# Optimization experiments

Measured on AMD Instinct MI355X. Metric: run time of the kernel, lower is better.

## Reference

```python
import jax, jax.numpy as jnp
import numpy as np

B, S = 128, 4096            # batch, num memory slots
W_NUM = 10000               # word_num (vocab)
CONT, FEAT, LSTM = 256, 256, 256
AH, CH = 128, 128           # actor/critic hidden dims
EPS = 1e-8


def _lin(key, out_d, in_d):
    k1, k2 = jax.random.split(key)
    s = 1.0 / np.sqrt(in_d)
    W = jax.random.uniform(k1, (out_d, in_d), jnp.float32, -s, s)
    b = jax.random.uniform(k2, (out_d,), jnp.float32, -s, s)
    return W, b


def setup_inputs() -> dict:
    key = jax.random.key(0)
    ks = jax.random.split(key, 18)
    d = {}
    d['x'] = jax.random.normal(ks[0], (B, W_NUM), jnp.float32)
    d['feat'] = jax.random.normal(ks[1], (B, S, FEAT), jnp.float32)
    d['h_tm1'] = jax.random.normal(ks[2], (B, LSTM), jnp.float32)
    d['c_tm1'] = jax.random.normal(ks[3], (B, LSTM), jnp.float32)
    d['W_x2cont'], d['b_x2cont'] = _lin(ks[4], CONT, W_NUM)
    d['W_h2cont'], d['b_h2cont'] = _lin(ks[5], CONT, LSTM)
    d['W_cont2key'], d['b_cont2key'] = _lin(ks[6], FEAT, CONT)
    d['W_cont2strength'], d['b_cont2strength'] = _lin(ks[7], 1, CONT)
    d['W_att_gates'], d['b_att_gates'] = _lin(ks[8], 1, FEAT + LSTM + CONT)
    d['W_ih'], d['b_ih'] = _lin(ks[9], 4 * LSTM, CONT + FEAT)
    d['W_hh'], d['b_hh'] = _lin(ks[10], 4 * LSTM, LSTM)
    d['W_actor_hid'], d['b_actor_hid'] = _lin(ks[11], AH, LSTM)
    d['W_critic_hid'], d['b_critic_hid'] = _lin(ks[12], CH, LSTM)
    d['W_actor'], d['b_actor'] = _lin(ks[13], W_NUM, AH)
    d['W_critic'], d['b_critic'] = _lin(ks[14], 1, CH)
    return d


def reference(x, feat, h_tm1, c_tm1,
              W_x2cont, b_x2cont, W_h2cont, b_h2cont,
              W_cont2key, b_cont2key, W_cont2strength, b_cont2strength,
              W_att_gates, b_att_gates, W_ih, b_ih, W_hh, b_hh,
              W_actor_hid, b_actor_hid, W_critic_hid, b_critic_hid,
              W_actor, b_actor, W_critic, b_critic):
    lin = lambda v, W, b: v @ W.T + b
    # controller
    x_cont = lin(x, W_x2cont, b_x2cont)                      # [B, CONT]
    h_cont = lin(h_tm1, W_h2cont, b_h2cont)                  # [B, CONT]
    control = jax.nn.relu(x_cont + h_cont)
    key_v = jnp.tanh(lin(control, W_cont2key, b_cont2key))   # [B, FEAT]
    strength = jax.nn.relu(lin(control, W_cont2strength, b_cont2strength)) + 1.0  # [B,1]
    # NTM-style content addressing: sharpened cosine similarity -> softmax over slots
    feat_n = jnp.linalg.norm(feat, axis=-1)                  # [B, S]
    key_n = jnp.linalg.norm(key_v, axis=-1, keepdims=True)   # [B, 1]
    sim = jnp.einsum('bsd,bd->bs', feat, key_v) / (feat_n * key_n + EPS)
    alpha = jax.nn.softmax(strength * sim, axis=-1)          # [B, S]
    cand_att_vec = jnp.einsum('bs,bsd->bd', alpha, feat)     # [B, FEAT]
    # attention gate
    gate_in = jnp.concatenate([cand_att_vec, h_tm1, x_cont], axis=1)  # [B, FEAT+LSTM+CONT]
    gates_att = jax.nn.sigmoid(lin(gate_in, W_att_gates, b_att_gates))
    att_vec = cand_att_vec * gates_att
    # LSTM cell (PyTorch gate order: i, f, g, o)
    inp_lstm = jnp.concatenate([att_vec, x_cont], axis=1)    # [B, FEAT+CONT]
    g = lin(inp_lstm, W_ih, b_ih) + lin(h_tm1, W_hh, b_hh)
    i, f, gg, o = jnp.split(g, 4, axis=1)
    c = jax.nn.sigmoid(f) * c_tm1 + jax.nn.sigmoid(i) * jnp.tanh(gg)
    h = jax.nn.sigmoid(o) * jnp.tanh(c)
    # heads
    action_logit = lin(jax.nn.relu(lin(h, W_actor_hid, b_actor_hid)), W_actor, b_actor)
    value = lin(jax.nn.relu(lin(h, W_critic_hid, b_critic_hid)), W_critic, b_critic)
    return (action_logit, value, h, c)
```

## Files before the change

kernel.cpp:

```cpp
#include <hip/hip_runtime.h>
#include <cmath>


#define B_ 128
#define S_ 4096
#define WN 10000
#define CD 256

__global__ __launch_bounds__(256) void k1_xcont(
    const float* __restrict__ x, const float* __restrict__ Wx,
    float* __restrict__ part) {
  const int nt = blockIdx.x;
  const int ks = blockIdx.y;
  const int t = threadIdx.x;
  __shared__ float4 xs[128][16];
  __shared__ float4 wsW[16][16];
  const int o0 = nt * 16;
  const int og = t & 3;
  const int bg = t >> 2;
  const int bgx = bg & 7;
  float acc[2][4] = {{0.f, 0.f, 0.f, 0.f}, {0.f, 0.f, 0.f, 0.f}};
  for (int sub = 0; sub < 4; ++sub) {
    const int k0 = ks * 256 + sub * 64;
    for (int q = t; q < 2048; q += 256) {
      const int row = q >> 4, c4 = q & 15;
      const int k = k0 + c4 * 4;
      float4 v = make_float4(0.f, 0.f, 0.f, 0.f);
      if (k < WN) v = *(const float4*)(x + (size_t)row * WN + k);
      xs[row][c4 ^ (row & 7)] = v;
    }
    {
      const int row = t >> 4, c4 = t & 15;
      const int k = k0 + c4 * 4;
      float4 v = make_float4(0.f, 0.f, 0.f, 0.f);
      if (k < WN) v = *(const float4*)(Wx + (size_t)(o0 + row) * WN + k);
      wsW[row][c4 ^ (row & 7)] = v;
    }
    __syncthreads();
#pragma unroll
    for (int c4 = 0; c4 < 16; ++c4) {
      float4 wv[4];
#pragma unroll
      for (int i = 0; i < 4; ++i) wv[i] = wsW[og * 4 + i][c4 ^ ((og * 4 + i) & 7)];
#pragma unroll
      for (int j = 0; j < 2; ++j) {
        const float4 xv = xs[bg + j * 64][c4 ^ bgx];
#pragma unroll
        for (int i = 0; i < 4; ++i)
          acc[j][i] += xv.x * wv[i].x + xv.y * wv[i].y + xv.z * wv[i].z + xv.w * wv[i].w;
      }
    }
    __syncthreads();
  }
#pragma unroll
  for (int j = 0; j < 2; ++j) {
    const int bb = bg + j * 64;
#pragma unroll
    for (int i = 0; i < 4; ++i)
      part[(size_t)ks * 32768 + bb * 256 + o0 + og * 4 + i] = acc[j][i];
  }
}

__global__ __launch_bounds__(256) void k2_controller(
    const float* __restrict__ part, const float* __restrict__ bx,
    const float* __restrict__ h_tm1, const float* __restrict__ Wh,
    const float* __restrict__ bh, const float* __restrict__ Wk,
    const float* __restrict__ bk, const float* __restrict__ Ws,
    const float* __restrict__ bs, float* __restrict__ x_cont,
    float* __restrict__ key_v, float* __restrict__ strength,
    float* __restrict__ key_n) {
  const int b = blockIdx.x, t = threadIdx.x;
  __shared__ float hs[256], cs[256];
  __shared__ float r1[4], r2[4];
  hs[t] = h_tm1[b * 256 + t];
  float xc = bx[t];
  for (int ks = 0; ks < 40; ++ks) xc += part[(size_t)ks * 32768 + b * 256 + t];
  x_cont[b * 256 + t] = xc;
  __syncthreads();
  float hc = bh[t];
  {
    const float* w = Wh + (size_t)t * 256;
    for (int k = 0; k < 256; k += 4) {
      float4 wv = *(const float4*)(w + k);
      hc += hs[k] * wv.x + hs[k + 1] * wv.y + hs[k + 2] * wv.z + hs[k + 3] * wv.w;
    }
  }
  const float ctl = fmaxf(xc + hc, 0.f);
  cs[t] = ctl;
  __syncthreads();
  float kvv = bk[t];
  {
    const float* w = Wk + (size_t)t * 256;
    for (int k = 0; k < 256; k += 4) {
      float4 wv = *(const float4*)(w + k);
      kvv += cs[k] * wv.x + cs[k + 1] * wv.y + cs[k + 2] * wv.z + cs[k + 3] * wv.w;
    }
  }
  kvv = tanhf(kvv);
  key_v[b * 256 + t] = kvv;
  float v1 = kvv * kvv;
  float v2 = ctl * Ws[t];
  for (int off = 32; off; off >>= 1) {
    v1 += __shfl_xor(v1, off);
    v2 += __shfl_xor(v2, off);
  }
  const int w_ = t >> 6, lane = t & 63;
  if (lane == 0) { r1[w_] = v1; r2[w_] = v2; }
  __syncthreads();
  if (t == 0) {
    const float n2 = r1[0] + r1[1] + r1[2] + r1[3];
    const float sd = r2[0] + r2[1] + r2[2] + r2[3];
    key_n[b] = sqrtf(n2);
    strength[b] = fmaxf(sd + bs[0], 0.f) + 1.f;
  }
}

__global__ __launch_bounds__(256, 4) void k3_attn(
    const float* __restrict__ feat, const float* __restrict__ key_v,
    const float* __restrict__ strength, const float* __restrict__ key_n,
    float* __restrict__ att_part) {
  const int ss = blockIdx.x;
  const int b = blockIdx.y;
  const int t = threadIdx.x;
  const int w = t >> 6, lane = t & 63;
  const int g = lane >> 4;
  const int l = lane & 15;
  const float str = strength[b];
  const float kn = key_n[b];
  float4 kf[4];
#pragma unroll
  for (int p = 0; p < 4; ++p)
    kf[p] = *(const float4*)(key_v + b * 256 + p * 64 + l * 4);
  const float* fb = feat + ((size_t)b * S_ + (size_t)ss * 256 + (size_t)w * 64) * 256;
  const float* fl = fb + (size_t)g * 256 + l * 4;
  float4 o[4];
#pragma unroll
  for (int p = 0; p < 4; ++p) o[p] = make_float4(0.f, 0.f, 0.f, 0.f);
  float lsum = 0.f;
  float4 fC[4], fN[4];
#pragma unroll
  for (int p = 0; p < 4; ++p) fC[p] = *(const float4*)(fl + p * 64);
#pragma unroll 2
  for (int r = 0; r < 16; ++r) {
    if (r < 15) {
      const float* fr = fl + (size_t)(r + 1) * 1024;
#pragma unroll
      for (int p = 0; p < 4; ++p) fN[p] = *(const float4*)(fr + p * 64);
    }
    float d = 0.f, n2 = 0.f;
#pragma unroll
    for (int p = 0; p < 4; ++p) {
      d  += fC[p].x * kf[p].x + fC[p].y * kf[p].y + fC[p].z * kf[p].z + fC[p].w * kf[p].w;
      n2 += fC[p].x * fC[p].x + fC[p].y * fC[p].y + fC[p].z * fC[p].z + fC[p].w * fC[p].w;
    }
#pragma unroll
    for (int off = 8; off; off >>= 1) {
      d  += __shfl_xor(d, off);
      n2 += __shfl_xor(n2, off);
    }
    const float sc = str * d / (sqrtf(n2) * kn + 1e-8f);
    const float a = __expf(sc - str);
    lsum += a;
#pragma unroll
    for (int p = 0; p < 4; ++p) {
      o[p].x += a * fC[p].x; o[p].y += a * fC[p].y;
      o[p].z += a * fC[p].z; o[p].w += a * fC[p].w;
    }
#pragma unroll
    for (int p = 0; p < 4; ++p) fC[p] = fN[p];
  }
#pragma unroll
  for (int off = 16; off <= 32; off <<= 1) {
    lsum += __shfl_xor(lsum, off);
#pragma unroll
    for (int p = 0; p < 4; ++p) {
      o[p].x += __shfl_xor(o[p].x, off);
      o[p].y += __shfl_xor(o[p].y, off);
      o[p].z += __shfl_xor(o[p].z, off);
      o[p].w += __shfl_xor(o[p].w, off);
    }
  }
  __shared__ float wo[4][256];
  __shared__ float wl[4];
  if (g == 0) {
#pragma unroll
    for (int p = 0; p < 4; ++p) *(float4*)&wo[w][p * 64 + l * 4] = o[p];
    if (l == 0) wl[w] = lsum;
  }
  __syncthreads();
  const float od = wo[0][t] + wo[1][t] + wo[2][t] + wo[3][t];
  float* apo = att_part + (size_t)(b * 16 + ss) * 264;
  if (t == 0) apo[0] = wl[0] + wl[1] + wl[2] + wl[3];
  apo[4 + t] = od;
}

__global__ __launch_bounds__(256) void k4a_gate(
    const float* __restrict__ att_part, const float* __restrict__ h_tm1,
    const float* __restrict__ x_cont, const float* __restrict__ Wg,
    const float* __restrict__ bg_, float* __restrict__ inp_cat) {
  const int b = blockIdx.x, t = threadIdx.x;
  const float* ap = att_part + (size_t)b * 16 * 264;
  float lg = 0.f, od = 0.f;
#pragma unroll
  for (int ss = 0; ss < 16; ++ss) {
    lg += ap[ss * 264];
    od += ap[ss * 264 + 4 + t];
  }
  const float cand = od / lg;
  const float hv = h_tm1[b * 256 + t];
  const float xc = x_cont[b * 256 + t];
  float v = cand * Wg[t] + hv * Wg[256 + t] + xc * Wg[512 + t];
  for (int off = 32; off; off >>= 1) v += __shfl_xor(v, off);
  __shared__ float rr[4];
  __shared__ float gsh;
  const int w_ = t >> 6, lane = t & 63;
  if (lane == 0) rr[w_] = v;
  __syncthreads();
  if (t == 0) {
    const float s = rr[0] + rr[1] + rr[2] + rr[3] + bg_[0];
    gsh = 1.f / (1.f + expf(-s));
  }
  __syncthreads();
  inp_cat[b * 768 + t] = cand * gsh;
  inp_cat[b * 768 + 256 + t] = xc;
  inp_cat[b * 768 + 512 + t] = hv;
}

__global__ __launch_bounds__(256) void k4b_lstm(
    const float* __restrict__ inp_cat, const float* __restrict__ Wih,
    const float* __restrict__ bih, const float* __restrict__ Whh,
    const float* __restrict__ bhh, const float* __restrict__ c_tm1,
    float* __restrict__ h_out, float* __restrict__ c_out) {
  const int j0 = blockIdx.x * 2;
  const int t = threadIdx.x;
  __shared__ float inp_s[128][132];
  __shared__ float w_s[8][132];
  const int b = t >> 1, half = t & 1;
  float acc[4] = {0.f, 0.f, 0.f, 0.f};
  for (int kc = 0; kc < 6; ++kc) {
    const int kbase = kc * 128;
    for (int q = t; q < 4096; q += 256) {
      const int row = q >> 5, c4 = q & 31;
      *(float4*)&inp_s[row][c4 * 4] =
          *(const float4*)(inp_cat + (size_t)row * 768 + kbase + c4 * 4);
    }
    {
      const int row = t >> 5, c4 = t & 31;
      const int gate = row & 3;
      const int j = j0 + (row >> 2);
      const int og = gate * 256 + j;
      const int kg = kbase + c4 * 4;
      float4 v;
      if (kg < 512) v = *(const float4*)(Wih + (size_t)og * 512 + kg);
      else          v = *(const float4*)(Whh + (size_t)og * 256 + (kg - 512));
      *(float4*)&w_s[row][c4 * 4] = v;
    }
    __syncthreads();
    for (int k = 0; k < 128; k += 4) {
      const float4 iv = *(const float4*)&inp_s[b][k];
#pragma unroll
      for (int g = 0; g < 4; ++g) {
        const float4 wv = *(const float4*)&w_s[half * 4 + g][k];
        acc[g] += iv.x * wv.x + iv.y * wv.y + iv.z * wv.z + iv.w * wv.w;
      }
    }
    __syncthreads();
  }
  const int j = j0 + half;
  const float gi = acc[0] + bih[j] + bhh[j];
  const float gf = acc[1] + bih[256 + j] + bhh[256 + j];
  const float gg = acc[2] + bih[512 + j] + bhh[512 + j];
  const float go = acc[3] + bih[768 + j] + bhh[768 + j];
  const float ct = c_tm1[b * 256 + j];
  const float i_ = 1.f / (1.f + expf(-gi));
  const float f_ = 1.f / (1.f + expf(-gf));
  const float g_ = tanhf(gg);
  const float o_ = 1.f / (1.f + expf(-go));
  const float c = f_ * ct + i_ * g_;
  const float h = o_ * tanhf(c);
  h_out[b * 256 + j] = h;
  c_out[b * 256 + j] = c;
}

__global__ __launch_bounds__(256) void k5_hid(
    const float* __restrict__ h_in, const float* __restrict__ Wah,
    const float* __restrict__ bah, const float* __restrict__ Wch,
    const float* __restrict__ bch, float* __restrict__ hidA,
    float* __restrict__ hidC) {
  const int b = blockIdx.x, t = threadIdx.x;
  __shared__ float hs[256];
  hs[t] = h_in[b * 256 + t];
  __syncthreads();
  const float* W = (t < 128) ? (Wah + (size_t)t * 256) : (Wch + (size_t)(t - 128) * 256);
  float s = (t < 128) ? bah[t] : bch[t - 128];
  for (int k = 0; k < 256; k += 4) {
    const float4 w = *(const float4*)(W + k);
    s += hs[k] * w.x + hs[k + 1] * w.y + hs[k + 2] * w.z + hs[k + 3] * w.w;
  }
  s = fmaxf(s, 0.f);
  if (t < 128) hidA[b * 128 + t] = s;
  else         hidC[b * 128 + (t - 128)] = s;
}

__global__ __launch_bounds__(256) void k6_heads(
    const float* __restrict__ hidA, const float* __restrict__ hidC,
    const float* __restrict__ Wa, const float* __restrict__ ba,
    const float* __restrict__ Wc, const float* __restrict__ bc,
    float* __restrict__ logits, float* __restrict__ value) {
  const int t = threadIdx.x;
  const int bx = blockIdx.x, by = blockIdx.y;
  if (bx == 157) {
    if (by == 0 && t < 128) {
      const float* hc = hidC + (size_t)t * 128;
      float s = bc[0];
      for (int k = 0; k < 128; k += 4) {
        const float4 w = *(const float4*)(Wc + k);
        s += hc[k] * w.x + hc[k + 1] * w.y + hc[k + 2] * w.z + hc[k + 3] * w.w;
      }
      value[t] = s;
    }
    return;
  }
  const int o0 = bx * 64;
  const int b0 = by * 32;
  __shared__ float4 ha[32][32];
  __shared__ float4 wa[64][32];
  for (int q = t; q < 1024; q += 256) {
    const int row = q >> 5, c4 = q & 31;
    ha[row][c4 ^ ((row >> 2) & 7)] =
        *(const float4*)(hidA + (size_t)(b0 + row) * 128 + c4 * 4);
  }
  for (int q = t; q < 2048; q += 256) {
    const int row = q >> 5, c4 = q & 31;
    const int o = o0 + row;
    float4 v = make_float4(0.f, 0.f, 0.f, 0.f);
    if (o < WN) v = *(const float4*)(Wa + (size_t)o * 128 + c4 * 4);
    wa[row][c4 ^ ((row >> 2) & 7)] = v;
  }
  __syncthreads();
  const int og = t & 15, bq = t >> 4;
  float acc[2][4];
#pragma unroll
  for (int r = 0; r < 2; ++r)
#pragma unroll
    for (int i = 0; i < 4; ++i) acc[r][i] = 0.f;
#pragma unroll 4
  for (int c4 = 0; c4 < 32; ++c4) {
    float4 wv[4];
#pragma unroll
    for (int i = 0; i < 4; ++i) wv[i] = wa[og * 4 + i][c4 ^ (og & 7)];
#pragma unroll
    for (int r = 0; r < 2; ++r) {
      const int row = bq * 2 + r;
      const float4 hv = ha[row][c4 ^ ((row >> 2) & 7)];
#pragma unroll
      for (int i = 0; i < 4; ++i)
        acc[r][i] += hv.x * wv[i].x + hv.y * wv[i].y + hv.z * wv[i].z + hv.w * wv[i].w;
    }
  }
  const int obase = o0 + og * 4;
#pragma unroll
  for (int r = 0; r < 2; ++r) {
    const int bb = b0 + bq * 2 + r;
    if (obase + 3 < WN) {
      const float4 bias = *(const float4*)(ba + obase);
      float4 res;
      res.x = acc[r][0] + bias.x;
      res.y = acc[r][1] + bias.y;
      res.z = acc[r][2] + bias.z;
      res.w = acc[r][3] + bias.w;
      *(float4*)(logits + (size_t)bb * WN + obase) = res;
    } else {
      for (int i = 0; i < 4; ++i)
        if (obase + i < WN) logits[(size_t)bb * WN + obase + i] = acc[r][i] + ba[obase + i];
    }
  }
}

extern "C" void kernel_launch(void* const* d_in, const int* in_sizes, int n_in,
                              void* d_out, int out_size, void* d_ws, size_t ws_size,
                              hipStream_t stream) {
  const float* x     = (const float*)d_in[0];
  const float* feat  = (const float*)d_in[1];
  const float* h_tm1 = (const float*)d_in[2];
  const float* c_tm1 = (const float*)d_in[3];
  const float* Wx2c  = (const float*)d_in[4];
  const float* bx2c  = (const float*)d_in[5];
  const float* Wh2c  = (const float*)d_in[6];
  const float* bh2c  = (const float*)d_in[7];
  const float* Wc2k  = (const float*)d_in[8];
  const float* bc2k  = (const float*)d_in[9];
  const float* Wc2s  = (const float*)d_in[10];
  const float* bc2s  = (const float*)d_in[11];
  const float* Wag   = (const float*)d_in[12];
  const float* bag   = (const float*)d_in[13];
  const float* Wih   = (const float*)d_in[14];
  const float* bih   = (const float*)d_in[15];
  const float* Whh   = (const float*)d_in[16];
  const float* bhh   = (const float*)d_in[17];
  const float* Wah   = (const float*)d_in[18];
  const float* bah   = (const float*)d_in[19];
  const float* Wch   = (const float*)d_in[20];
  const float* bch   = (const float*)d_in[21];
  const float* Wa    = (const float*)d_in[22];
  const float* ba    = (const float*)d_in[23];
  const float* Wc    = (const float*)d_in[24];
  const float* bc    = (const float*)d_in[25];

  float* out    = (float*)d_out;
  float* logits = out;
  float* value  = out + 1280000;
  float* h_out  = out + 1280128;
  float* c_out  = out + 1312896;

  float* wsf      = (float*)d_ws;
  float* part     = wsf;
  float* x_cont   = part + 1310720;
  float* key_v    = x_cont + 32768;
  float* strength = key_v + 32768;
  float* key_n    = strength + 128;
  float* att_part = key_n + 128;
  float* inp_cat  = att_part + 540672;
  float* hidA     = inp_cat + 98304;
  float* hidC     = hidA + 16384;

  k1_xcont<<<dim3(16, 40), 256, 0, stream>>>(x, Wx2c, part);
  k2_controller<<<128, 256, 0, stream>>>(part, bx2c, h_tm1, Wh2c, bh2c,
                                         Wc2k, bc2k, Wc2s, bc2s,
                                         x_cont, key_v, strength, key_n);
  k3_attn<<<dim3(16, 128), 256, 0, stream>>>(feat, key_v, strength, key_n, att_part);
  k4a_gate<<<128, 256, 0, stream>>>(att_part, h_tm1, x_cont, Wag, bag, inp_cat);
  k4b_lstm<<<128, 256, 0, stream>>>(inp_cat, Wih, bih, Whh, bhh, c_tm1, h_out, c_out);
  k5_hid<<<128, 256, 0, stream>>>(h_out, Wah, bah, Wch, bch, hidA, hidC);
  k6_heads<<<dim3(158, 4), 256, 0, stream>>>(hidA, hidC, Wa, ba, Wc, bc, logits, value);
}
```

Before: 284.6 us.

## Split attention over more slot chunks, use DPP reductions, fully unroll feat loop

The attention kernel now processes 128 slots per block instead of 256, doubling the grid to 32x128 blocks, and the gate kernel sums 32 partials instead of 16. The per-row loop is fully unrolled with double-buffered float4 loads, split accumulators, and DPP row_shr-based 16-lane reductions in place of shuffles. This aims to raise memory-level parallelism and cut reduction latency on the bandwidth-bound feat stream (512 MB). It costs a larger partial buffer and more combine work. The DPP reduction leaves the full sum only in the highest lane of each 16-lane row, which may be inconsistent with how other lanes use it.

Measured after the change: 563.8 us. 98.1% more time.

```diff
diff --git a/kernel.cpp b/kernel.cpp
--- a/kernel.cpp
+++ b/kernel.cpp
@@ -115,6 +115,19 @@
   }
 }
 
+__device__ __forceinline__ float dpp_add16(float x) {
+  int t;
+  t = __builtin_amdgcn_update_dpp(0, __float_as_int(x), 0x121, 0xf, 0xf, true);
+  x += __int_as_float(t);
+  t = __builtin_amdgcn_update_dpp(0, __float_as_int(x), 0x122, 0xf, 0xf, true);
+  x += __int_as_float(t);
+  t = __builtin_amdgcn_update_dpp(0, __float_as_int(x), 0x124, 0xf, 0xf, true);
+  x += __int_as_float(t);
+  t = __builtin_amdgcn_update_dpp(0, __float_as_int(x), 0x128, 0xf, 0xf, true);
+  x += __int_as_float(t);
+  return x;
+}
+
 __global__ __launch_bounds__(256, 4) void k3_attn(
     const float* __restrict__ feat, const float* __restrict__ key_v,
     const float* __restrict__ strength, const float* __restrict__ key_n,
@@ -131,44 +144,69 @@
 #pragma unroll
   for (int p = 0; p < 4; ++p)
     kf[p] = *(const float4*)(key_v + b * 256 + p * 64 + l * 4);
-  const float* fb = feat + ((size_t)b * S_ + (size_t)ss * 256 + (size_t)w * 64) * 256;
+  const float* fb = feat + ((size_t)b * S_ + (size_t)ss * 128 + (size_t)w * 32) * 256;
   const float* fl = fb + (size_t)g * 256 + l * 4;
   float4 o[4];
 #pragma unroll
   for (int p = 0; p < 4; ++p) o[p] = make_float4(0.f, 0.f, 0.f, 0.f);
   float lsum = 0.f;
-  float4 fC[4], fN[4];
-#pragma unroll
-  for (int p = 0; p < 4; ++p) fC[p] = *(const float4*)(fl + p * 64);
-#pragma unroll 2
-  for (int r = 0; r < 16; ++r) {
-    if (r < 15) {
-      const float* fr = fl + (size_t)(r + 1) * 1024;
-#pragma unroll
-      for (int p = 0; p < 4; ++p) fN[p] = *(const float4*)(fr + p * 64);
-    }
-    float d = 0.f, n2 = 0.f;
-#pragma unroll
-    for (int p = 0; p < 4; ++p) {
-      d  += fC[p].x * kf[p].x + fC[p].y * kf[p].y + fC[p].z * kf[p].z + fC[p].w * kf[p].w;
-      n2 += fC[p].x * fC[p].x + fC[p].y * fC[p].y + fC[p].z * fC[p].z + fC[p].w * fC[p].w;
-    }
-#pragma unroll
-    for (int off = 8; off; off >>= 1) {
-      d  += __shfl_xor(d, off);
-      n2 += __shfl_xor(n2, off);
-    }
-    const float sc = str * d / (sqrtf(n2) * kn + 1e-8f);
-    const float a = __expf(sc - str);
-    lsum += a;
-#pragma unroll
-    for (int p = 0; p < 4; ++p) {
-      o[p].x += a * fC[p].x; o[p].y += a * fC[p].y;
-      o[p].z += a * fC[p].z; o[p].w += a * fC[p].w;
-    }
-#pragma unroll
-    for (int p = 0; p < 4; ++p) fC[p] = fN[p];
-  }
+  float4 fA[4], fB[4];
+
+#define LOADQ(dst, q)                                                       \
+  {                                                                         \
+    const float* fr_ = fl + (size_t)(q) * 1024;                             \
+    dst[0] = *(const float4*)(fr_);                                         \
+    dst[1] = *(const float4*)(fr_ + 64);                                    \
+    dst[2] = *(const float4*)(fr_ + 128);                                   \
+    dst[3] = *(const float4*)(fr_ + 192);                                   \
+  }
+
+#define PROCQ(f)                                                            \
+  {                                                                         \
+    float dp0 = f[0].x * kf[0].x, nn0 = f[0].x * f[0].x;                    \
+    float dp1 = f[1].x * kf[1].x, nn1 = f[1].x * f[1].x;                    \
+    float dp2 = f[2].x * kf[2].x, nn2 = f[2].x * f[2].x;                    \
+    float dp3 = f[3].x * kf[3].x, nn3 = f[3].x * f[3].x;                    \
+    dp0 += f[0].y * kf[0].y; nn0 += f[0].y * f[0].y;                        \
+    dp1 += f[1].y * kf[1].y; nn1 += f[1].y * f[1].y;                        \
+    dp2 += f[2].y * kf[2].y; nn2 += f[2].y * f[2].y;                        \
+    dp3 += f[3].y * kf[3].y; nn3 += f[3].y * f[3].y;                        \
+    dp0 += f[0].z * kf[0].z; nn0 += f[0].z * f[0].z;                        \
+    dp1 += f[1].z * kf[1].z; nn1 += f[1].z * f[1].z;                        \
+    dp2 += f[2].z * kf[2].z; nn2 += f[2].z * f[2].z;                        \
+    dp3 += f[3].z * kf[3].z; nn3 += f[3].z * f[3].z;                        \
+    dp0 += f[0].w * kf[0].w; nn0 += f[0].w * f[0].w;                        \
+    dp1 += f[1].w * kf[1].w; nn1 += f[1].w * f[1].w;                        \
+    dp2 += f[2].w * kf[2].w; nn2 += f[2].w * f[2].w;                        \
+    dp3 += f[3].w * kf[3].w; nn3 += f[3].w * f[3].w;                        \
+    float d = (dp0 + dp1) + (dp2 + dp3);                                    \
+    float n2 = (nn0 + nn1) + (nn2 + nn3);                                   \
+    d = dpp_add16(d);                                                       \
+    n2 = dpp_add16(n2);                                                     \
+    const float sc = str * d / (sqrtf(n2) * kn + 1e-8f);                    \
+    const float a = __expf(sc - str);                                       \
+    lsum += a;                                                              \
+    o[0].x += a * f[0].x; o[0].y += a * f[0].y;                             \
+    o[0].z += a * f[0].z; o[0].w += a * f[0].w;                             \
+    o[1].x += a * f[1].x; o[1].y += a * f[1].y;                             \
+    o[1].z += a * f[1].z; o[1].w += a * f[1].w;                             \
+    o[2].x += a * f[2].x; o[2].y += a * f[2].y;                             \
+    o[2].z += a * f[2].z; o[2].w += a * f[2].w;                             \
+    o[3].x += a * f[3].x; o[3].y += a * f[3].y;                             \
+    o[3].z += a * f[3].z; o[3].w += a * f[3].w;                             \
+  }
+
+  LOADQ(fA, 0);
+#pragma unroll
+  for (int rr = 0; rr < 4; ++rr) {
+    LOADQ(fB, 2 * rr + 1);
+    PROCQ(fA);
+    if (rr < 3) LOADQ(fA, 2 * rr + 2);
+    PROCQ(fB);
+  }
+#undef LOADQ
+#undef PROCQ
+
 #pragma unroll
   for (int off = 16; off <= 32; off <<= 1) {
     lsum += __shfl_xor(lsum, off);
@@ -189,7 +227,7 @@
   }
   __syncthreads();
   const float od = wo[0][t] + wo[1][t] + wo[2][t] + wo[3][t];
-  float* apo = att_part + (size_t)(b * 16 + ss) * 264;
+  float* apo = att_part + (size_t)(b * 32 + ss) * 264;
   if (t == 0) apo[0] = wl[0] + wl[1] + wl[2] + wl[3];
   apo[4 + t] = od;
 }
@@ -199,10 +237,10 @@
     const float* __restrict__ x_cont, const float* __restrict__ Wg,
     const float* __restrict__ bg_, float* __restrict__ inp_cat) {
   const int b = blockIdx.x, t = threadIdx.x;
-  const float* ap = att_part + (size_t)b * 16 * 264;
+  const float* ap = att_part + (size_t)b * 32 * 264;
   float lg = 0.f, od = 0.f;
 #pragma unroll
-  for (int ss = 0; ss < 16; ++ss) {
+  for (int ss = 0; ss < 32; ++ss) {
     lg += ap[ss * 264];
     od += ap[ss * 264 + 4 + t];
   }
@@ -420,7 +458,7 @@
   float* strength = key_v + 32768;
   float* key_n    = strength + 128;
   float* att_part = key_n + 128;
-  float* inp_cat  = att_part + 540672;
+  float* inp_cat  = att_part + 1081344;
   float* hidA     = inp_cat + 98304;
   float* hidC     = hidA + 16384;
 
@@ -428,7 +466,7 @@
   k2_controller<<<128, 256, 0, stream>>>(part, bx2c, h_tm1, Wh2c, bh2c,
                                          Wc2k, bc2k, Wc2s, bc2s,
                                          x_cont, key_v, strength, key_n);
-  k3_attn<<<dim3(16, 128), 256, 0, stream>>>(feat, key_v, strength, key_n, att_part);
+  k3_attn<<<dim3(32, 128), 256, 0, stream>>>(feat, key_v, strength, key_n, att_part);
   k4a_gate<<<128, 256, 0, stream>>>(att_part, h_tm1, x_cont, Wag, bag, inp_cat);
   k4b_lstm<<<128, 256, 0, stream>>>(inp_cat, Wih, bih, Whh, bhh, c_tm1, h_out, c_out);
   k5_hid<<<128, 256, 0, stream>>>(h_out, Wah, bah, Wch, bch, hidA, hidC);
```

## Stream feat through double-buffered LDS via global_load_lds in attention kernel

Applied to the files above, without the earlier changes.

Rewrites the attention kernel so each block stages 32-row tiles of feat into shared memory with async global-to-LDS loads, double-buffered, then computes similarity and weighted sum from LDS. Each block now covers 1024 slots instead of 256, so the grid shrinks from 16x128 to 4x128 and there are fewer partial results to reduce in the gate kernel. The goal is to keep more feat bytes in flight and take the prefetch out of registers. The trade-off is 64KB of LDS per block, which limits occupancy, plus a barrier after every tile.

New measurement: 273.4 us. 1.04x faster.

```diff
diff --git a/kernel.cpp b/kernel.cpp
--- a/kernel.cpp
+++ b/kernel.cpp
@@ -115,7 +115,7 @@
   }
 }
 
-__global__ __launch_bounds__(256, 4) void k3_attn(
+__global__ __launch_bounds__(256) void k3_attn(
     const float* __restrict__ feat, const float* __restrict__ key_v,
     const float* __restrict__ strength, const float* __restrict__ key_n,
     float* __restrict__ att_part) {
@@ -125,50 +125,77 @@
   const int w = t >> 6, lane = t & 63;
   const int g = lane >> 4;
   const int l = lane & 15;
+
+  __shared__ __align__(16) float tile[2][32][256];
+  __shared__ float wl[4];
+
   const float str = strength[b];
   const float kn = key_n[b];
   float4 kf[4];
 #pragma unroll
   for (int p = 0; p < 4; ++p)
     kf[p] = *(const float4*)(key_v + b * 256 + p * 64 + l * 4);
-  const float* fb = feat + ((size_t)b * S_ + (size_t)ss * 256 + (size_t)w * 64) * 256;
-  const float* fl = fb + (size_t)g * 256 + l * 4;
+
+  const float* fbase = feat + ((size_t)b * S_ + (size_t)ss * 1024) * 256;
+
+  auto stage = [&](int nt, int buf) {
+#pragma unroll
+    for (int j = 0; j < 8; ++j) {
+      const int row = w * 8 + j;
+      const float* gp = fbase + ((size_t)nt * 32 + row) * 256 + lane * 4;
+      float* lp = &tile[buf][row][0];
+      __builtin_amdgcn_global_load_lds(
+          (const __attribute__((address_space(1))) void*)gp,
+          (__attribute__((address_space(3))) void*)lp, 16, 0, 0);
+    }
+  };
+
   float4 o[4];
 #pragma unroll
   for (int p = 0; p < 4; ++p) o[p] = make_float4(0.f, 0.f, 0.f, 0.f);
   float lsum = 0.f;
-  float4 fC[4], fN[4];
-#pragma unroll
-  for (int p = 0; p < 4; ++p) fC[p] = *(const float4*)(fl + p * 64);
-#pragma unroll 2
-  for (int r = 0; r < 16; ++r) {
-    if (r < 15) {
-      const float* fr = fl + (size_t)(r + 1) * 1024;
-#pragma unroll
-      for (int p = 0; p < 4; ++p) fN[p] = *(const float4*)(fr + p * 64);
-    }
-    float d = 0.f, n2 = 0.f;
-#pragma unroll
-    for (int p = 0; p < 4; ++p) {
-      d  += fC[p].x * kf[p].x + fC[p].y * kf[p].y + fC[p].z * kf[p].z + fC[p].w * kf[p].w;
-      n2 += fC[p].x * fC[p].x + fC[p].y * fC[p].y + fC[p].z * fC[p].z + fC[p].w * fC[p].w;
-    }
-#pragma unroll
-    for (int off = 8; off; off >>= 1) {
-      d  += __shfl_xor(d, off);
-      n2 += __shfl_xor(n2, off);
-    }
-    const float sc = str * d / (sqrtf(n2) * kn + 1e-8f);
-    const float a = __expf(sc - str);
-    lsum += a;
-#pragma unroll
-    for (int p = 0; p < 4; ++p) {
-      o[p].x += a * fC[p].x; o[p].y += a * fC[p].y;
-      o[p].z += a * fC[p].z; o[p].w += a * fC[p].w;
-    }
-#pragma unroll
-    for (int p = 0; p < 4; ++p) fC[p] = fN[p];
-  }
+
+  const int NT = 32;
+  stage(0, 0);
+#pragma unroll 1
+  for (int nt = 0; nt < NT; ++nt) {
+    const int buf = nt & 1;
+    if (nt + 1 < NT) stage(nt + 1, buf ^ 1);
+    if (nt == 0) __syncthreads();
+#pragma unroll
+    for (int qq = 0; qq < 2; ++qq) {
+      const int row = 4 * w + 16 * qq + g;
+      const float* rp = &tile[buf][row][l * 4];
+      const float4 f0 = *(const float4*)(rp);
+      const float4 f1 = *(const float4*)(rp + 64);
+      const float4 f2 = *(const float4*)(rp + 128);
+      const float4 f3 = *(const float4*)(rp + 192);
+      float dp0 = f0.x * kf[0].x + f0.y * kf[0].y + f0.z * kf[0].z + f0.w * kf[0].w;
+      float dp1 = f1.x * kf[1].x + f1.y * kf[1].y + f1.z * kf[1].z + f1.w * kf[1].w;
+      float dp2 = f2.x * kf[2].x + f2.y * kf[2].y + f2.z * kf[2].z + f2.w * kf[2].w;
+      float dp3 = f3.x * kf[3].x + f3.y * kf[3].y + f3.z * kf[3].z + f3.w * kf[3].w;
+      float nn0 = f0.x * f0.x + f0.y * f0.y + f0.z * f0.z + f0.w * f0.w;
+      float nn1 = f1.x * f1.x + f1.y * f1.y + f1.z * f1.z + f1.w * f1.w;
+      float nn2 = f2.x * f2.x + f2.y * f2.y + f2.z * f2.z + f2.w * f2.w;
+      float nn3 = f3.x * f3.x + f3.y * f3.y + f3.z * f3.z + f3.w * f3.w;
+      float d = (dp0 + dp1) + (dp2 + dp3);
+      float n2 = (nn0 + nn1) + (nn2 + nn3);
+#pragma unroll
+      for (int off = 8; off; off >>= 1) {
+        d += __shfl_xor(d, off);
+        n2 += __shfl_xor(n2, off);
+      }
+      const float sc = str * d / (sqrtf(n2) * kn + 1e-8f);
+      const float a = __expf(sc - str);
+      lsum += a;
+      o[0].x += a * f0.x; o[0].y += a * f0.y; o[0].z += a * f0.z; o[0].w += a * f0.w;
+      o[1].x += a * f1.x; o[1].y += a * f1.y; o[1].z += a * f1.z; o[1].w += a * f1.w;
+      o[2].x += a * f2.x; o[2].y += a * f2.y; o[2].z += a * f2.z; o[2].w += a * f2.w;
+      o[3].x += a * f3.x; o[3].y += a * f3.y; o[3].z += a * f3.z; o[3].w += a * f3.w;
+    }
+    __syncthreads();
+  }
+
 #pragma unroll
   for (int off = 16; off <= 32; off <<= 1) {
     lsum += __shfl_xor(lsum, off);
@@ -180,8 +207,7 @@
       o[p].w += __shfl_xor(o[p].w, off);
     }
   }
-  __shared__ float wo[4][256];
-  __shared__ float wl[4];
+  float (*wo)[256] = (float (*)[256]) & tile[0][0][0];
   if (g == 0) {
 #pragma unroll
     for (int p = 0; p < 4; ++p) *(float4*)&wo[w][p * 64 + l * 4] = o[p];
@@ -189,7 +215,7 @@
   }
   __syncthreads();
   const float od = wo[0][t] + wo[1][t] + wo[2][t] + wo[3][t];
-  float* apo = att_part + (size_t)(b * 16 + ss) * 264;
+  float* apo = att_part + (size_t)(b * 4 + ss) * 264;
   if (t == 0) apo[0] = wl[0] + wl[1] + wl[2] + wl[3];
   apo[4 + t] = od;
 }
@@ -199,10 +225,10 @@
     const float* __restrict__ x_cont, const float* __restrict__ Wg,
     const float* __restrict__ bg_, float* __restrict__ inp_cat) {
   const int b = blockIdx.x, t = threadIdx.x;
-  const float* ap = att_part + (size_t)b * 16 * 264;
+  const float* ap = att_part + (size_t)b * 4 * 264;
   float lg = 0.f, od = 0.f;
 #pragma unroll
-  for (int ss = 0; ss < 16; ++ss) {
+  for (int ss = 0; ss < 4; ++ss) {
     lg += ap[ss * 264];
     od += ap[ss * 264 + 4 + t];
   }
@@ -420,7 +446,7 @@
   float* strength = key_v + 32768;
   float* key_n    = strength + 128;
   float* att_part = key_n + 128;
-  float* inp_cat  = att_part + 540672;
+  float* inp_cat  = att_part + 135168;
   float* hidA     = inp_cat + 98304;
   float* hidC     = hidA + 16384;
 
@@ -428,7 +454,7 @@
   k2_controller<<<128, 256, 0, stream>>>(part, bx2c, h_tm1, Wh2c, bh2c,
                                          Wc2k, bc2k, Wc2s, bc2s,
                                          x_cont, key_v, strength, key_n);
-  k3_attn<<<dim3(16, 128), 256, 0, stream>>>(feat, key_v, strength, key_n, att_part);
+  k3_attn<<<dim3(4, 128), 256, 0, stream>>>(feat, key_v, strength, key_n, att_part);
   k4a_gate<<<128, 256, 0, stream>>>(att_part, h_tm1, x_cont, Wag, bag, inp_cat);
   k4b_lstm<<<128, 256, 0, stream>>>(inp_cat, Wih, bih, Whh, bhh, c_tm1, h_out, c_out);
   k5_hid<<<128, 256, 0, stream>>>(h_out, Wah, bah, Wch, bch, hidA, hidC);
```

## Stream attention feat tiles through LDS with async multi-stage global_load_lds pipeline

Applied to the files above, without the earlier changes.

Rewrites the attention kernel so each block covers 1024 slots instead of 256. Feature rows are fetched with asynchronous global-to-LDS loads into a 4-deep ring buffer, and explicit vmcnt waits overlap the loads with the dot-product and accumulate work. Partial results per batch drop from 16 to 4, and the gate kernel and workspace offsets are updated to match. The aim is to keep more memory requests in flight on the bandwidth-bound feat read. The cost is 64KB+ of LDS per block, which lowers occupancy, and a grid four times smaller.

New measurement: 273.0 us. -4.1%, faster.

```diff
diff --git a/kernel.cpp b/kernel.cpp
--- a/kernel.cpp
+++ b/kernel.cpp
@@ -115,7 +115,7 @@
   }
 }
 
-__global__ __launch_bounds__(256, 4) void k3_attn(
+__global__ __launch_bounds__(256) void k3_attn(
     const float* __restrict__ feat, const float* __restrict__ key_v,
     const float* __restrict__ strength, const float* __restrict__ key_n,
     float* __restrict__ att_part) {
@@ -125,50 +125,86 @@
   const int w = t >> 6, lane = t & 63;
   const int g = lane >> 4;
   const int l = lane & 15;
+
+  __shared__ __align__(16) float tile[4][16][256];
+  __shared__ float wo[4][256];
+  __shared__ float wl[4];
+
   const float str = strength[b];
   const float kn = key_n[b];
   float4 kf[4];
 #pragma unroll
   for (int p = 0; p < 4; ++p)
     kf[p] = *(const float4*)(key_v + b * 256 + p * 64 + l * 4);
-  const float* fb = feat + ((size_t)b * S_ + (size_t)ss * 256 + (size_t)w * 64) * 256;
-  const float* fl = fb + (size_t)g * 256 + l * 4;
+
+  const float* fbase = feat + ((size_t)b * S_ + (size_t)ss * 1024) * 256;
+
+#define STAGE(nt, buf)                                                        \
+  {                                                                           \
+    _Pragma("unroll") for (int j = 0; j < 4; ++j) {                           \
+      const int row_ = w * 4 + j;                                             \
+      const float* gp_ = fbase + ((size_t)(nt)*16 + row_) * 256 + lane * 4;   \
+      __builtin_amdgcn_global_load_lds(                                       \
+          (const __attribute__((address_space(1))) void*)gp_,                 \
+          (__attribute__((address_space(3))) void*)&tile[buf][row_][0], 16,   \
+          0, 0);                                                              \
+    }                                                                         \
+  }
+
   float4 o[4];
 #pragma unroll
   for (int p = 0; p < 4; ++p) o[p] = make_float4(0.f, 0.f, 0.f, 0.f);
   float lsum = 0.f;
-  float4 fC[4], fN[4];
-#pragma unroll
-  for (int p = 0; p < 4; ++p) fC[p] = *(const float4*)(fl + p * 64);
-#pragma unroll 2
-  for (int r = 0; r < 16; ++r) {
-    if (r < 15) {
-      const float* fr = fl + (size_t)(r + 1) * 1024;
-#pragma unroll
-      for (int p = 0; p < 4; ++p) fN[p] = *(const float4*)(fr + p * 64);
-    }
-    float d = 0.f, n2 = 0.f;
-#pragma unroll
-    for (int p = 0; p < 4; ++p) {
-      d  += fC[p].x * kf[p].x + fC[p].y * kf[p].y + fC[p].z * kf[p].z + fC[p].w * kf[p].w;
-      n2 += fC[p].x * fC[p].x + fC[p].y * fC[p].y + fC[p].z * fC[p].z + fC[p].w * fC[p].w;
-    }
-#pragma unroll
-    for (int off = 8; off; off >>= 1) {
-      d  += __shfl_xor(d, off);
-      n2 += __shfl_xor(n2, off);
-    }
-    const float sc = str * d / (sqrtf(n2) * kn + 1e-8f);
-    const float a = __expf(sc - str);
-    lsum += a;
-#pragma unroll
-    for (int p = 0; p < 4; ++p) {
-      o[p].x += a * fC[p].x; o[p].y += a * fC[p].y;
-      o[p].z += a * fC[p].z; o[p].w += a * fC[p].w;
-    }
-#pragma unroll
-    for (int p = 0; p < 4; ++p) fC[p] = fN[p];
-  }
+
+#define COMPUTE(buf)                                                          \
+  {                                                                           \
+    const int row_ = w * 4 + g;                                               \
+    const float* rp_ = &tile[buf][row_][l * 4];                               \
+    const float4 f0 = *(const float4*)(rp_);                                  \
+    const float4 f1 = *(const float4*)(rp_ + 64);                             \
+    const float4 f2 = *(const float4*)(rp_ + 128);                            \
+    const float4 f3 = *(const float4*)(rp_ + 192);                            \
+    float dp0 = f0.x * kf[0].x + f0.y * kf[0].y + f0.z * kf[0].z + f0.w * kf[0].w; \
+    float dp1 = f1.x * kf[1].x + f1.y * kf[1].y + f1.z * kf[1].z + f1.w * kf[1].w; \
+    float dp2 = f2.x * kf[2].x + f2.y * kf[2].y + f2.z * kf[2].z + f2.w * kf[2].w; \
+    float dp3 = f3.x * kf[3].x + f3.y * kf[3].y + f3.z * kf[3].z + f3.w * kf[3].w; \
+    float nn0 = f0.x * f0.x + f0.y * f0.y + f0.z * f0.z + f0.w * f0.w;        \
+    float nn1 = f1.x * f1.x + f1.y * f1.y + f1.z * f1.z + f1.w * f1.w;        \
+    float nn2 = f2.x * f2.x + f2.y * f2.y + f2.z * f2.z + f2.w * f2.w;        \
+    float nn3 = f3.x * f3.x + f3.y * f3.y + f3.z * f3.z + f3.w * f3.w;        \
+    float d_ = (dp0 + dp1) + (dp2 + dp3);                                     \
+    float n2_ = (nn0 + nn1) + (nn2 + nn3);                                    \
+    _Pragma("unroll") for (int off = 8; off; off >>= 1) {                     \
+      d_ += __shfl_xor(d_, off);                                              \
+      n2_ += __shfl_xor(n2_, off);                                            \
+    }                                                                         \
+    const float sc_ = str * d_ / (sqrtf(n2_) * kn + 1e-8f);                   \
+    const float a_ = __expf(sc_ - str);                                       \
+    lsum += a_;                                                               \
+    o[0].x += a_ * f0.x; o[0].y += a_ * f0.y; o[0].z += a_ * f0.z; o[0].w += a_ * f0.w; \
+    o[1].x += a_ * f1.x; o[1].y += a_ * f1.y; o[1].z += a_ * f1.z; o[1].w += a_ * f1.w; \
+    o[2].x += a_ * f2.x; o[2].y += a_ * f2.y; o[2].z += a_ * f2.z; o[2].w += a_ * f2.w; \
+    o[3].x += a_ * f3.x; o[3].y += a_ * f3.y; o[3].z += a_ * f3.z; o[3].w += a_ * f3.w; \
+  }
+
+  STAGE(0, 0);
+  STAGE(1, 1);
+  STAGE(2, 2);
+#pragma unroll 1
+  for (int nt = 0; nt < 61; ++nt) {
+    asm volatile("s_waitcnt vmcnt(8)" ::: "memory");
+    STAGE(nt + 3, (nt + 3) & 3);
+    COMPUTE(nt & 3);
+  }
+  asm volatile("s_waitcnt vmcnt(8)" ::: "memory");
+  COMPUTE(1);
+  asm volatile("s_waitcnt vmcnt(4)" ::: "memory");
+  COMPUTE(2);
+  asm volatile("s_waitcnt vmcnt(0)" ::: "memory");
+  COMPUTE(3);
+#undef STAGE
+#undef COMPUTE
+
 #pragma unroll
   for (int off = 16; off <= 32; off <<= 1) {
     lsum += __shfl_xor(lsum, off);
@@ -180,8 +216,6 @@
       o[p].w += __shfl_xor(o[p].w, off);
     }
   }
-  __shared__ float wo[4][256];
-  __shared__ float wl[4];
   if (g == 0) {
 #pragma unroll
     for (int p = 0; p < 4; ++p) *(float4*)&wo[w][p * 64 + l * 4] = o[p];
@@ -189,7 +223,7 @@
   }
   __syncthreads();
   const float od = wo[0][t] + wo[1][t] + wo[2][t] + wo[3][t];
-  float* apo = att_part + (size_t)(b * 16 + ss) * 264;
+  float* apo = att_part + (size_t)(b * 4 + ss) * 264;
   if (t == 0) apo[0] = wl[0] + wl[1] + wl[2] + wl[3];
   apo[4 + t] = od;
 }
@@ -199,10 +233,10 @@
     const float* __restrict__ x_cont, const float* __restrict__ Wg,
     const float* __restrict__ bg_, float* __restrict__ inp_cat) {
   const int b = blockIdx.x, t = threadIdx.x;
-  const float* ap = att_part + (size_t)b * 16 * 264;
+  const float* ap = att_part + (size_t)b * 4 * 264;
   float lg = 0.f, od = 0.f;
 #pragma unroll
-  for (int ss = 0; ss < 16; ++ss) {
+  for (int ss = 0; ss < 4; ++ss) {
     lg += ap[ss * 264];
     od += ap[ss * 264 + 4 + t];
   }
@@ -420,7 +454,7 @@
   float* strength = key_v + 32768;
   float* key_n    = strength + 128;
   float* att_part = key_n + 128;
-  float* inp_cat  = att_part + 540672;
+  float* inp_cat  = att_part + 135168;
   float* hidA     = inp_cat + 98304;
   float* hidC     = hidA + 16384;
 
@@ -428,7 +462,7 @@
   k2_controller<<<128, 256, 0, stream>>>(part, bx2c, h_tm1, Wh2c, bh2c,
                                          Wc2k, bc2k, Wc2s, bc2s,
                                          x_cont, key_v, strength, key_n);
-  k3_attn<<<dim3(16, 128), 256, 0, stream>>>(feat, key_v, strength, key_n, att_part);
+  k3_attn<<<dim3(4, 128), 256, 0, stream>>>(feat, key_v, strength, key_n, att_part);
   k4a_gate<<<128, 256, 0, stream>>>(att_part, h_tm1, x_cont, Wag, bag, inp_cat);
   k4b_lstm<<<128, 256, 0, stream>>>(inp_cat, Wih, bih, Whh, bhh, c_tm1, h_out, c_out);
   k5_hid<<<128, 256, 0, stream>>>(h_out, Wah, bah, Wch, bch, hidA, hidC);
```
